# Optimization experiments

Measured on AMD Instinct MI355X. Metric: run time of the kernel, lower is better.

Reference implementation:

```python
import jax, jax.numpy as jnp
import numpy as np

N = 50000        # N_particles
E = 800000       # edges (avg degree 16)
SD = 32          # state_dim = 3 + 2*2 + 25
OC = 16          # message_out_channels
H = 32           # MLP hidden_channels
BN_EPS = 1e-5


def _bn(h, g, b):
    # PyG MLP default BatchNorm1d, training-mode batch stats over rows
    m = h.mean(axis=0)
    v = h.var(axis=0)
    return (h - m) * jax.lax.rsqrt(v + BN_EPS) * g + b


def _mlp3(h, w1, b1, g1, be1, w2, b2, g2, be2, w3, b3):
    # Linear -> BN -> ReLU, Linear -> BN -> ReLU, Linear
    h = jax.nn.relu(_bn(h @ w1 + b1, g1, be1))
    h = jax.nn.relu(_bn(h @ w2 + b2, g2, be2))
    return h @ w3 + b3


def setup_inputs() -> dict:
    key = jax.random.key(0)
    ks = jax.random.split(key, 16)

    def rn(k, shape):
        fan_in = shape[0] if len(shape) > 1 else shape[0]
        return jax.random.normal(k, shape, jnp.float32) / np.sqrt(fan_in)

    inp = {
        "x": jax.random.normal(ks[0], (N, SD), jnp.float32),
        "edge_attr": jax.random.normal(ks[1], (E, SD), jnp.float32),
        "edge_index": jax.random.randint(ks[2], (2, E), 0, N, jnp.int64),
        # edge-weight-generating MLP: SD -> 32 -> 32 -> SD*OC
        "msg_w1": rn(ks[3], (SD, H)), "msg_b1": jnp.zeros((H,), jnp.float32),
        "msg_g1": jnp.ones((H,), jnp.float32), "msg_be1": jnp.zeros((H,), jnp.float32),
        "msg_w2": rn(ks[4], (H, H)), "msg_b2": jnp.zeros((H,), jnp.float32),
        "msg_g2": jnp.ones((H,), jnp.float32), "msg_be2": jnp.zeros((H,), jnp.float32),
        "msg_w3": rn(ks[5], (H, SD * OC)), "msg_b3": jnp.zeros((SD * OC,), jnp.float32),
        # NNConv root weight + bias
        "root_w": rn(ks[6], (SD, OC)), "root_b": jnp.zeros((OC,), jnp.float32),
        # own_state_nn MLP: (SD+OC) -> 32 -> 32 -> SD
        "own_w1": rn(ks[7], (SD + OC, H)), "own_b1": jnp.zeros((H,), jnp.float32),
        "own_g1": jnp.ones((H,), jnp.float32), "own_be1": jnp.zeros((H,), jnp.float32),
        "own_w2": rn(ks[8], (H, H)), "own_b2": jnp.zeros((H,), jnp.float32),
        "own_g2": jnp.ones((H,), jnp.float32), "own_be2": jnp.zeros((H,), jnp.float32),
        "own_w3": rn(ks[9], (H, SD)), "own_b3": jnp.zeros((SD,), jnp.float32),
    }
    return inp


def reference(x, edge_attr, edge_index,
              msg_w1, msg_b1, msg_g1, msg_be1, msg_w2, msg_b2, msg_g2, msg_be2,
              msg_w3, msg_b3, root_w, root_b,
              own_w1, own_b1, own_g1, own_be1, own_w2, own_b2, own_g2, own_be2,
              own_w3, own_b3):
    src, dst = edge_index[0], edge_index[1]
    # per-edge weight matrices: [E, SD, OC]
    W_e = _mlp3(edge_attr, msg_w1, msg_b1, msg_g1, msg_be1,
                msg_w2, msg_b2, msg_g2, msg_be2, msg_w3, msg_b3)
    W_e = W_e.reshape(-1, SD, OC)
    # gather-matmul-scatter (NNConv, aggr='add')
    msg = jnp.einsum('ei,eio->eo', x[src], W_e)          # [E, OC]
    agg = jax.ops.segment_sum(msg, dst, num_segments=N)  # [N, OC]
    messages = agg + x @ root_w + root_b                 # root weight + bias
    combined = jnp.concatenate([x, messages], axis=-1)   # [N, SD+OC]
    new_state = _mlp3(combined, own_w1, own_b1, own_g1, own_be1,
                      own_w2, own_b2, own_g2, own_be2, own_w3, own_b3)
    return new_state
```

## Files before the change

### kernel.cpp

```cpp
#include <hip/hip_runtime.h>
#include <hip/hip_fp16.h>


#define N_NODES 50000
#define N_EDGES 800000
#define SD 32
#define OC 16
#define HID 32
#define BN_EPS 1e-5f
#define NTILES 196

#define OFF_STATS 0u
#define OFF_DEGS  5376u
#define OFF_CURS  205376u
#define OFF_DEGD  405376u
#define OFF_CURD  605376u
#define OFF_BASES 805376u
#define OFF_BASED 1005440u
#define OFF_POSS  1205504u
#define OFF_COMBO 4405504u
#define OFF_AGG   7605504u
#define OFF_H2S   10805504u
#define OFF_MSGB  62005504u

typedef _Float16 f16x8 __attribute__((ext_vector_type(8)));
typedef float f32x16 __attribute__((ext_vector_type(16)));

__device__ __forceinline__ float f4get(const float4& v, int ii) {
  return ii == 0 ? v.x : ii == 1 ? v.y : ii == 2 ? v.z : v.w;
}

__device__ __forceinline__ unsigned pack2(float a, float b) {
  __half2 h = __floats2half2_rn(a, b);
  return *reinterpret_cast<unsigned*>(&h);
}
__device__ __forceinline__ void unpk8(uint4 u, float* o) {
  __half2 a = *reinterpret_cast<__half2*>(&u.x), b = *reinterpret_cast<__half2*>(&u.y);
  __half2 c = *reinterpret_cast<__half2*>(&u.z), d = *reinterpret_cast<__half2*>(&u.w);
  float2 fa = __half22float2(a), fb = __half22float2(b);
  float2 fc = __half22float2(c), fd = __half22float2(d);
  o[0] = fa.x; o[1] = fa.y; o[2] = fb.x; o[3] = fb.y;
  o[4] = fc.x; o[5] = fc.y; o[6] = fd.x; o[7] = fd.y;
}

template<int I4, int IOFF>
__device__ __forceinline__ void mv_acc(const float4* __restrict__ rp,
                                       const float* __restrict__ wlds,
                                       float z[HID]) {
#pragma unroll
  for (int i4 = 0; i4 < I4; ++i4) {
    float4 rv = rp[i4];
#pragma unroll
    for (int ii = 0; ii < 4; ++ii) {
      float s = f4get(rv, ii);
      const float* wrow = wlds + (IOFF + i4 * 4 + ii) * HID;
#pragma unroll
      for (int h4 = 0; h4 < HID / 4; ++h4) {
        float4 wv = *reinterpret_cast<const float4*>(wrow + h4 * 4);
        z[h4 * 4 + 0] = fmaf(s, wv.x, z[h4 * 4 + 0]);
        z[h4 * 4 + 1] = fmaf(s, wv.y, z[h4 * 4 + 1]);
        z[h4 * 4 + 2] = fmaf(s, wv.z, z[h4 * 4 + 2]);
        z[h4 * 4 + 3] = fmaf(s, wv.w, z[h4 * 4 + 3]);
      }
    }
  }
}

__device__ __forceinline__ void mv_reg(const float* __restrict__ v,
                                       const float* __restrict__ wlds,
                                       float z[HID]) {
#pragma unroll
  for (int h = 0; h < HID; ++h) z[h] = 0.f;
#pragma unroll
  for (int i = 0; i < HID; ++i) {
    float s = v[i];
    const float* wrow = wlds + i * HID;
#pragma unroll
    for (int h4 = 0; h4 < HID / 4; ++h4) {
      float4 wv = *reinterpret_cast<const float4*>(wrow + h4 * 4);
      z[h4 * 4 + 0] = fmaf(s, wv.x, z[h4 * 4 + 0]);
      z[h4 * 4 + 1] = fmaf(s, wv.y, z[h4 * 4 + 1]);
      z[h4 * 4 + 2] = fmaf(s, wv.z, z[h4 * 4 + 2]);
      z[h4 * 4 + 3] = fmaf(s, wv.w, z[h4 * 4 + 3]);
    }
  }
}

__device__ __forceinline__ void bn_params(const float* __restrict__ stats, int off,
                                          float cntInv, const float* __restrict__ g,
                                          const float* __restrict__ be,
                                          float* __restrict__ sc, float* __restrict__ sf) {
  if (threadIdx.x < HID) {
    int h = threadIdx.x;
    float mean = stats[off + h] * cntInv;
    float var = stats[off + HID + h] * cntInv - mean * mean;
    float s = g[h] * rsqrtf(var + BN_EPS);
    sc[h] = s;
    sf[h] = fmaf(-mean, s, be[h]);
  }
}

__device__ __forceinline__ void tile_accum(const float z[HID], float* __restrict__ tile,
                                           int h, int g, float& s, float& q) {
  int tid = threadIdx.x;
  __syncthreads();
#pragma unroll
  for (int j = 0; j < HID; ++j) tile[tid * 33 + j] = z[j];
  __syncthreads();
#pragma unroll
  for (int k = 0; k < 32; ++k) {
    float v = tile[(g * 32 + k) * 33 + h];
    s += v;
    q = fmaf(v, v, q);
  }
}

__device__ __forceinline__ void tile_finish(float* __restrict__ tile, int h, int g,
                                            float s, float q,
                                            float* __restrict__ gstats) {
  int tid = threadIdx.x;
  __syncthreads();
  tile[g * 32 + h] = s;
  tile[256 + g * 32 + h] = q;
  __syncthreads();
  if (tid < 64) {
    int hh = tid & 31;
    int base = (tid < 32) ? 0 : 256;
    float acc = 0.f;
#pragma unroll
    for (int g2 = 0; g2 < 8; ++g2) acc += tile[base + g2 * 32 + hh];
    atomicAdd(gstats + ((tid < 32) ? hh : (HID + hh)), acc);
  }
}

__global__ __launch_bounds__(256) void kH(const int* __restrict__ ei,
                                          int* __restrict__ degS, int* __restrict__ degD) {
  int e = blockIdx.x * 256 + threadIdx.x;
  atomicAdd(degS + ei[e], 1);
  atomicAdd(degD + ei[N_EDGES + e], 1);
}

__global__ __launch_bounds__(1024) void kScan(const int* __restrict__ degS, int* __restrict__ baseS,
                                              const int* __restrict__ degD, int* __restrict__ baseD) {
  __shared__ int sc[1024];
  const int* deg = (blockIdx.x == 0) ? degS : degD;
  int* base = (blockIdx.x == 0) ? baseS : baseD;
  int t = threadIdx.x;
  const int C = 49;
  int st = t * C;
  int sum = 0;
  for (int k = 0; k < C; ++k) {
    int i = st + k;
    if (i < N_NODES) sum += deg[i];
  }
  sc[t] = sum;
  __syncthreads();
  for (int s = 1; s < 1024; s <<= 1) {
    int v = (t >= s) ? sc[t - s] : 0;
    __syncthreads();
    sc[t] += v;
    __syncthreads();
  }
  int run = sc[t] - sum;
  for (int k = 0; k < C; ++k) {
    int i = st + k;
    if (i < N_NODES) { base[i] = run; run += deg[i]; }
  }
  if (t == 1023) base[N_NODES] = run;
}

__global__ __launch_bounds__(256) void kRank(const int* __restrict__ ei,
    const int* __restrict__ baseS, const int* __restrict__ baseD,
    int* __restrict__ curS, int* __restrict__ curD,
    int* __restrict__ posS, unsigned* __restrict__ combo) {
  int e = blockIdx.x * 256 + threadIdx.x;
  int s = ei[e], d = ei[N_EDGES + e];
  int rs = atomicAdd(curS + s, 1);
  int ps = baseS[s] + rs;
  posS[e] = ps;
  int rd = atomicAdd(curD + d, 1);
  combo[ps] = (unsigned)(baseD[d] + rd) | ((unsigned)(s & 15) << 27);
}

template<int PHASE>
__global__ __launch_bounds__(256) void sE(
    const float* __restrict__ ea, const int* __restrict__ posS,
    const float* __restrict__ w1, const float* __restrict__ w2,
    const float* __restrict__ g1, const float* __restrict__ be1,
    float* __restrict__ stats, __half* __restrict__ h2s) {
  __shared__ _Float16 xpose[4][32 * 40];
  __shared__ float sred[4][2][32];
  int tid = threadIdx.x;
  int lane = tid & 63, wid = tid >> 6;
  int lr = lane & 31, lh = lane >> 5;

  f16x8 w1h[2], w1l[2], w2h[2], w2l[2];
#pragma unroll
  for (int kf = 0; kf < 2; ++kf) {
#pragma unroll
    for (int j = 0; j < 8; ++j) {
      int k = kf * 16 + lh * 8 + j;
      float v = w1[k * HID + lr];
      _Float16 hi = (_Float16)v;
      w1h[kf][j] = hi;
      w1l[kf][j] = (_Float16)(v - (float)hi);
      if (PHASE == 1) {
        float u = w2[k * HID + lr];
        _Float16 uh = (_Float16)u;
        w2h[kf][j] = uh;
        w2l[kf][j] = (_Float16)(u - (float)uh);
      } else {
        w2h[kf][j] = (_Float16)0.f;
        w2l[kf][j] = (_Float16)0.f;
      }
    }
  }
  float sc1 = 0.f, sf1 = 0.f;
  if (PHASE == 1) {
    float mean = stats[lr] * (1.f / N_EDGES);
    float var = stats[32 + lr] * (1.f / N_EDGES) - mean * mean;
    float s = g1[lr] * rsqrtf(var + BN_EPS);
    sc1 = s;
    sf1 = fmaf(-mean, s, be1[lr]);
  }
  float ssum = 0.f, ssq = 0.f;
  _Float16* xp = xpose[wid];

  for (int t = blockIdx.x * 4 + wid; t < N_EDGES / 32; t += gridDim.x * 4) {
    int e0 = t * 32;
    f16x8 ah[2], al[2];
#pragma unroll
    for (int kf = 0; kf < 2; ++kf) {
      const float4* p = reinterpret_cast<const float4*>(
          ea + (size_t)(e0 + lr) * SD + kf * 16 + lh * 8);
      float4 v0 = p[0], v1 = p[1];
      float vv[8] = {v0.x, v0.y, v0.z, v0.w, v1.x, v1.y, v1.z, v1.w};
#pragma unroll
      for (int j = 0; j < 8; ++j) {
        _Float16 hi = (_Float16)vv[j];
        ah[kf][j] = hi;
        al[kf][j] = (_Float16)(vv[j] - (float)hi);
      }
    }
    f32x16 acc = {};
#pragma unroll
    for (int kf = 0; kf < 2; ++kf) {
      acc = __builtin_amdgcn_mfma_f32_32x32x16_f16(ah[kf], w1h[kf], acc, 0, 0, 0);
      acc = __builtin_amdgcn_mfma_f32_32x32x16_f16(al[kf], w1h[kf], acc, 0, 0, 0);
      acc = __builtin_amdgcn_mfma_f32_32x32x16_f16(ah[kf], w1l[kf], acc, 0, 0, 0);
    }
    if (PHASE == 0) {
#pragma unroll
      for (int r = 0; r < 16; ++r) {
        ssum += acc[r];
        ssq = fmaf(acc[r], acc[r], ssq);
      }
    } else {
#pragma unroll
      for (int r = 0; r < 16; ++r) {
        int row = (r & 3) + 8 * (r >> 2) + 4 * lh;
        float h1 = fmaxf(0.f, fmaf(acc[r], sc1, sf1));
        xp[row * 40 + lr] = (_Float16)h1;
      }
      __builtin_amdgcn_sched_barrier(0);
      asm volatile("s_waitcnt lgkmcnt(0)" ::: "memory");
      __builtin_amdgcn_sched_barrier(0);
      f32x16 acc2 = {};
#pragma unroll
      for (int kf = 0; kf < 2; ++kf) {
        f16x8 a2 = *reinterpret_cast<const f16x8*>(xp + lr * 40 + kf * 16 + lh * 8);
        acc2 = __builtin_amdgcn_mfma_f32_32x32x16_f16(a2, w2h[kf], acc2, 0, 0, 0);
        acc2 = __builtin_amdgcn_mfma_f32_32x32x16_f16(a2, w2l[kf], acc2, 0, 0, 0);
      }
#pragma unroll
      for (int r = 0; r < 16; ++r) {
        ssum += acc2[r];
        ssq = fmaf(acc2[r], acc2[r], ssq);
      }
      __builtin_amdgcn_sched_barrier(0);
      asm volatile("s_waitcnt lgkmcnt(0)" ::: "memory");
      __builtin_amdgcn_sched_barrier(0);
#pragma unroll
      for (int r = 0; r < 16; ++r) {
        int row = (r & 3) + 8 * (r >> 2) + 4 * lh;
        xp[row * 40 + lr] = (_Float16)acc2[r];
      }
      __builtin_amdgcn_sched_barrier(0);
      asm volatile("s_waitcnt lgkmcnt(0)" ::: "memory");
      __builtin_amdgcn_sched_barrier(0);
      int ps = posS[e0 + lr];
      uint4 va = *reinterpret_cast<const uint4*>(xp + lr * 40 + lh * 16);
      uint4 vb = *reinterpret_cast<const uint4*>(xp + lr * 40 + lh * 16 + 8);
      __half* dst = (__half*)h2s + (size_t)ps * HID + lh * 16;
      *reinterpret_cast<uint4*>(dst) = va;
      *reinterpret_cast<uint4*>(dst + 8) = vb;
      __builtin_amdgcn_sched_barrier(0);
    }
  }
  ssum += __shfl_xor(ssum, 32);
  ssq += __shfl_xor(ssq, 32);
  if (lane < 32) {
    sred[wid][0][lane] = ssum;
    sred[wid][1][lane] = ssq;
  }
  __syncthreads();
  if (tid < 64) {
    int h = tid & 31, part = tid >> 5;
    float a = sred[0][part][h] + sred[1][part][h] + sred[2][part][h] + sred[3][part][h];
    atomicAdd(stats + (PHASE == 0 ? 0 : 64) + part * 32 + h, a);
  }
}

__global__ __launch_bounds__(256) void k5_gemm(
    const float* __restrict__ x, const float* __restrict__ w3,
    const float* __restrict__ b3, const unsigned* __restrict__ combo,
    const int* __restrict__ baseS, const __half* __restrict__ h2s,
    const float* __restrict__ stats, const float* __restrict__ g2,
    const float* __restrict__ be2, __half* __restrict__ msgb) {
  __shared__ float Tl[16 * 516];
  __shared__ float xsl[16][33];
  __shared__ float xbl[256];
  __shared__ float b3s[SD * OC];
  __shared__ float sc2[HID], sf2[HID];
  __shared__ int jr[2];
  int tid = threadIdx.x;
  int n0 = blockIdx.x * 16;
  for (int f = tid; f < 16 * SD; f += 256)
    xsl[f >> 5][f & 31] = x[(size_t)n0 * SD + f];
  for (int f = tid; f < SD * OC; f += 256) b3s[f] = b3[f];
  if (tid == 0) jr[0] = baseS[n0];
  if (tid == 1) jr[1] = baseS[n0 + 16];
  bn_params(stats, 64, 1.f / N_EDGES, g2, be2, sc2, sf2);
  __syncthreads();
  {
    int nl = tid >> 4, o = tid & 15;
    float a1 = 0.f;
#pragma unroll
    for (int i = 0; i < SD; ++i) a1 = fmaf(xsl[nl][i], b3s[i * OC + o], a1);
    xbl[tid] = a1;
  }
  {
    int oH = tid & 1, hh = (tid >> 1) & 31, ng = tid >> 6;
    float acc[4][8];
#pragma unroll
    for (int k = 0; k < 4; ++k)
#pragma unroll
      for (int j = 0; j < 8; ++j) acc[k][j] = 0.f;
    const float* wbase = w3 + hh * (SD * OC) + oH * 8;
#pragma unroll
    for (int i = 0; i < SD; ++i) {
      float4 wa = *reinterpret_cast<const float4*>(wbase + i * OC);
      float4 wb = *reinterpret_cast<const float4*>(wbase + i * OC + 4);
#pragma unroll
      for (int k = 0; k < 4; ++k) {
        float xv = xsl[ng * 4 + k][i];
        acc[k][0] = fmaf(xv, wa.x, acc[k][0]);
        acc[k][1] = fmaf(xv, wa.y, acc[k][1]);
        acc[k][2] = fmaf(xv, wa.z, acc[k][2]);
        acc[k][3] = fmaf(xv, wa.w, acc[k][3]);
        acc[k][4] = fmaf(xv, wb.x, acc[k][4]);
        acc[k][5] = fmaf(xv, wb.y, acc[k][5]);
        acc[k][6] = fmaf(xv, wb.z, acc[k][6]);
        acc[k][7] = fmaf(xv, wb.w, acc[k][7]);
      }
    }
#pragma unroll
    for (int k = 0; k < 4; ++k)
#pragma unroll
      for (int jj = 0; jj < 8; ++jj)
        Tl[(ng * 4 + k) * 516 + (oH * 8 + jj) * 32 + hh] = acc[k][jj];
  }
  __syncthreads();
  int jbeg = jr[0], jend = jr[1];
  for (int j = jbeg + tid; j < jend; j += 256) {
    unsigned c = combo[j];
    int dp = (int)(c & 0x07FFFFFFu);
    int nl = (int)(c >> 27);
    const uint4* hp = reinterpret_cast<const uint4*>(h2s + (size_t)j * HID);
    uint4 u0 = hp[0], u1 = hp[1], u2 = hp[2], u3 = hp[3];
    float h2v[HID];
    unpk8(u0, h2v + 0); unpk8(u1, h2v + 8);
    unpk8(u2, h2v + 16); unpk8(u3, h2v + 24);
#pragma unroll
    for (int k = 0; k < HID; ++k) h2v[k] = fmaxf(0.f, fmaf(h2v[k], sc2[k], sf2[k]));
    float m[OC];
#pragma unroll
    for (int o = 0; o < OC; ++o) m[o] = xbl[nl * 16 + o];
#pragma unroll
    for (int o = 0; o < OC; ++o) {
      const float* tb = Tl + nl * 516 + o * 32;
      float a = m[o];
#pragma unroll
      for (int h4 = 0; h4 < 8; ++h4) {
        float4 t = *reinterpret_cast<const float4*>(tb + h4 * 4);
        a = fmaf(h2v[h4 * 4 + 0], t.x, a);
        a = fmaf(h2v[h4 * 4 + 1], t.y, a);
        a = fmaf(h2v[h4 * 4 + 2], t.z, a);
        a = fmaf(h2v[h4 * 4 + 3], t.w, a);
      }
      m[o] = a;
    }
    unsigned us[8];
#pragma unroll
    for (int q = 0; q < 8; ++q) us[q] = pack2(m[2 * q], m[2 * q + 1]);
    uint4* mp = reinterpret_cast<uint4*>(msgb + (size_t)dp * OC);
    mp[0] = make_uint4(us[0], us[1], us[2], us[3]);
    mp[1] = make_uint4(us[4], us[5], us[6], us[7]);
  }
}

__global__ __launch_bounds__(256) void k6_aggr_own(
    const int* __restrict__ baseD, const __half* __restrict__ msgb,
    const float* __restrict__ x, const float* __restrict__ rootw,
    const float* __restrict__ rootb, const float* __restrict__ ow1,
    float* __restrict__ agg, float* __restrict__ stats) {
  __shared__ float xsl[16][33];
  __shared__ float aggl[16 * 17];
  __shared__ float rws[SD * OC];
  __shared__ float ow1s[(SD + OC) * HID];
  __shared__ float zt[16 * 33];
  __shared__ float rbs[OC];
  int tid = threadIdx.x;
  int n0 = blockIdx.x * 16;
  for (int f = tid; f < 16 * SD; f += 256) xsl[f >> 5][f & 31] = x[(size_t)n0 * SD + f];
  for (int f = tid; f < SD * OC; f += 256) rws[f] = rootw[f];
  for (int f = tid; f < (SD + OC) * HID; f += 256) ow1s[f] = ow1[f];
  if (tid < OC) rbs[tid] = rootb[tid];
  __syncthreads();
  int nl = tid >> 4, o = tid & 15;
  int d = n0 + nl;
  float r = rbs[o];
#pragma unroll
  for (int i = 0; i < SD; ++i) r = fmaf(xsl[nl][i], rws[i * OC + o], r);
  int b0 = baseD[d], b1 = baseD[d + 1];
  float s = 0.f;
  for (int j = b0; j < b1; ++j) s += __half2float(msgb[(size_t)j * OC + o]);
  float val = r + s;
  agg[(size_t)d * OC + o] = val;
  aggl[nl * 17 + o] = val;
  __syncthreads();
  float za = 0.f, zb = 0.f;
#pragma unroll
  for (int i = 0; i < SD; ++i) {
    float xv = xsl[nl][i];
    za = fmaf(xv, ow1s[i * HID + o], za);
    zb = fmaf(xv, ow1s[i * HID + o + 16], zb);
  }
#pragma unroll
  for (int i = 0; i < OC; ++i) {
    float mv = aggl[nl * 17 + i];
    za = fmaf(mv, ow1s[(SD + i) * HID + o], za);
    zb = fmaf(mv, ow1s[(SD + i) * HID + o + 16], zb);
  }
  zt[nl * 33 + o] = za;
  zt[nl * 33 + o + 16] = zb;
  __syncthreads();
  if (tid < 64) {
    int h = tid & 31;
    bool issq = tid >= 32;
    float acc = 0.f;
#pragma unroll
    for (int k = 0; k < 16; ++k) {
      float v = zt[k * 33 + h];
      acc += issq ? v * v : v;
    }
    atomicAdd(stats + 128 + (issq ? 32 : 0) + h, acc);
  }
}

__global__ __launch_bounds__(256) void s2_own(
    const float* __restrict__ x, const float* __restrict__ msgs,
    const float* __restrict__ w1, const float* __restrict__ w2,
    const float* __restrict__ g1, const float* __restrict__ be1,
    float* __restrict__ stats) {
  __shared__ float w1s[(SD + OC) * HID], w2s[HID * HID];
  __shared__ float sc1[HID], sf1[HID];
  __shared__ float tile[256 * 33];
  for (int f = threadIdx.x; f < (SD + OC) * HID; f += 256) w1s[f] = w1[f];
  for (int f = threadIdx.x; f < HID * HID; f += 256) w2s[f] = w2[f];
  bn_params(stats, 128, 1.f / N_NODES, g1, be1, sc1, sf1);
  int h = threadIdx.x & 31, g = threadIdx.x >> 5;
  float s = 0.f, q = 0.f;
  __syncthreads();
#pragma unroll 1
  for (int t = blockIdx.x; t < NTILES; t += gridDim.x) {
    int n = t * 256 + threadIdx.x;
    float z2[HID];
#pragma unroll
    for (int j = 0; j < HID; ++j) z2[j] = 0.f;
    if (n < N_NODES) {
      const float4* xp = reinterpret_cast<const float4*>(x + (size_t)n * SD);
      const float4* mp = reinterpret_cast<const float4*>(msgs + (size_t)n * OC);
      float z1[HID];
#pragma unroll
      for (int j = 0; j < HID; ++j) z1[j] = 0.f;
      mv_acc<8, 0>(xp, w1s, z1);
      mv_acc<4, SD>(mp, w1s, z1);
#pragma unroll
      for (int i = 0; i < HID; ++i) z1[i] = fmaxf(0.f, fmaf(z1[i], sc1[i], sf1[i]));
      mv_reg(z1, w2s, z2);
    }
    tile_accum(z2, tile, h, g, s, q);
  }
  tile_finish(tile, h, g, s, q, stats + 192);
}

__global__ __launch_bounds__(256) void k10_own_out(
    const float* __restrict__ x, const float* __restrict__ msgs,
    const float* __restrict__ w1, const float* __restrict__ w2,
    const float* __restrict__ w3o, const float* __restrict__ b3o,
    const float* __restrict__ g1, const float* __restrict__ be1,
    const float* __restrict__ g2, const float* __restrict__ be2,
    const float* __restrict__ stats, float* __restrict__ out) {
  __shared__ float w1s[(SD + OC) * HID], w2s[HID * HID], w3s[HID * SD];
  __shared__ float sc1[HID], sf1[HID], sc2[HID], sf2[HID];
  for (int f = threadIdx.x; f < (SD + OC) * HID; f += 256) w1s[f] = w1[f];
  for (int f = threadIdx.x; f < HID * HID; f += 256) w2s[f] = w2[f];
  for (int f = threadIdx.x; f < HID * SD; f += 256) w3s[f] = w3o[f];
  bn_params(stats, 128, 1.f / N_NODES, g1, be1, sc1, sf1);
  bn_params(stats, 192, 1.f / N_NODES, g2, be2, sc2, sf2);
  __syncthreads();
  int n = blockIdx.x * 256 + threadIdx.x;
  if (n >= N_NODES) return;
  const float4* xp = reinterpret_cast<const float4*>(x + (size_t)n * SD);
  const float4* mp = reinterpret_cast<const float4*>(msgs + (size_t)n * OC);
  float z1[HID];
#pragma unroll
  for (int j = 0; j < HID; ++j) z1[j] = 0.f;
  mv_acc<8, 0>(xp, w1s, z1);
  mv_acc<4, SD>(mp, w1s, z1);
#pragma unroll
  for (int i = 0; i < HID; ++i) z1[i] = fmaxf(0.f, fmaf(z1[i], sc1[i], sf1[i]));
  float z2[HID];
  mv_reg(z1, w2s, z2);
#pragma unroll
  for (int i = 0; i < HID; ++i) z2[i] = fmaxf(0.f, fmaf(z2[i], sc2[i], sf2[i]));
  float z3[HID];
  mv_reg(z2, w3s, z3);
  float4* op = reinterpret_cast<float4*>(out + (size_t)n * SD);
#pragma unroll
  for (int j4 = 0; j4 < 8; ++j4) {
    op[j4] = make_float4(z3[j4 * 4 + 0] + b3o[j4 * 4 + 0],
                         z3[j4 * 4 + 1] + b3o[j4 * 4 + 1],
                         z3[j4 * 4 + 2] + b3o[j4 * 4 + 2],
                         z3[j4 * 4 + 3] + b3o[j4 * 4 + 3]);
  }
}

extern "C" void kernel_launch(void* const* d_in, const int* in_sizes, int n_in,
                              void* d_out, int out_size, void* d_ws, size_t ws_size,
                              hipStream_t stream) {
  const float* x    = (const float*)d_in[0];
  const float* ea   = (const float*)d_in[1];
  const int*   ei   = (const int*)d_in[2];
  const float* mw1  = (const float*)d_in[3];
  const float* mg1  = (const float*)d_in[5];
  const float* mbe1 = (const float*)d_in[6];
  const float* mw2  = (const float*)d_in[7];
  const float* mg2  = (const float*)d_in[9];
  const float* mbe2 = (const float*)d_in[10];
  const float* mw3  = (const float*)d_in[11];
  const float* mb3  = (const float*)d_in[12];
  const float* rw   = (const float*)d_in[13];
  const float* rb   = (const float*)d_in[14];
  const float* ow1  = (const float*)d_in[15];
  const float* og1  = (const float*)d_in[17];
  const float* obe1 = (const float*)d_in[18];
  const float* ow2  = (const float*)d_in[19];
  const float* og2  = (const float*)d_in[21];
  const float* obe2 = (const float*)d_in[22];
  const float* ow3  = (const float*)d_in[23];
  const float* ob3  = (const float*)d_in[24];
  float* out = (float*)d_out;

  char* ws = (char*)d_ws;
  float* stats    = (float*)(ws + OFF_STATS);
  int* degS       = (int*)(ws + OFF_DEGS);
  int* curS       = (int*)(ws + OFF_CURS);
  int* degD       = (int*)(ws + OFF_DEGD);
  int* curD       = (int*)(ws + OFF_CURD);
  int* baseS      = (int*)(ws + OFF_BASES);
  int* baseD      = (int*)(ws + OFF_BASED);
  int* posS       = (int*)(ws + OFF_POSS);
  unsigned* combo = (unsigned*)(ws + OFF_COMBO);
  float* agg      = (float*)(ws + OFF_AGG);
  __half* h2s     = (__half*)(ws + OFF_H2S);
  __half* msgb    = (__half*)(ws + OFF_MSGB);

  hipMemsetAsync(ws, 0, 805376, stream);

  kH<<<3125, 256, 0, stream>>>(ei, degS, degD);
  kScan<<<2, 1024, 0, stream>>>(degS, baseS, degD, baseD);
  kRank<<<3125, 256, 0, stream>>>(ei, baseS, baseD, curS, curD, posS, combo);
  sE<0><<<1024, 256, 0, stream>>>(ea, posS, mw1, mw2, mg1, mbe1, stats, h2s);
  sE<1><<<1024, 256, 0, stream>>>(ea, posS, mw1, mw2, mg1, mbe1, stats, h2s);
  k5_gemm<<<3125, 256, 0, stream>>>(x, mw3, mb3, combo, baseS, h2s,
                                    stats, mg2, mbe2, msgb);
  k6_aggr_own<<<3125, 256, 0, stream>>>(baseD, msgb, x, rw, rb, ow1, agg, stats);
  s2_own<<<NTILES, 256, 0, stream>>>(x, agg, ow1, ow2, og1, obe1, stats);
  k10_own_out<<<(N_NODES + 255) / 256, 256, 0, stream>>>(
      x, agg, ow1, ow2, ow3, ob3, og1, obe1, og2, obe2, stats, out);
}
```

Before: 733.0 us.

## Derive first BN stats from edge_attr Gram matrix; merge rank atomics into histogram pass

```diff
diff --git a/kernel.cpp b/kernel.cpp
--- a/kernel.cpp
+++ b/kernel.cpp
@@ -10,18 +10,20 @@
 #define BN_EPS 1e-5f
 #define NTILES 196
 
-#define OFF_STATS 0u
-#define OFF_DEGS  5376u
-#define OFF_CURS  205376u
-#define OFF_DEGD  405376u
-#define OFF_CURD  605376u
-#define OFF_BASES 805376u
-#define OFF_BASED 1005440u
-#define OFF_POSS  1205504u
-#define OFF_COMBO 4405504u
-#define OFF_AGG   7605504u
-#define OFF_H2S   10805504u
-#define OFF_MSGB  62005504u
+#define OFF_STATS   0u
+#define OFF_MA      1024u
+#define OFF_MB      5120u
+#define OFF_EASUM   9216u
+#define OFF_CURS    9728u
+#define OFF_CURD    209728u
+#define OFF_BASES   409728u
+#define OFF_BASED   609792u
+#define OFF_RANKS   809856u
+#define OFF_RKD_POS 4009856u
+#define OFF_COMBO   7209856u
+#define OFF_AGG     10409856u
+#define OFF_H2S     13609856u
+#define OFF_MSGB    64809856u
 
 typedef _Float16 f16x8 __attribute__((ext_vector_type(8)));
 typedef float f32x16 __attribute__((ext_vector_type(16)));
@@ -133,11 +135,13 @@
   }
 }
 
-__global__ __launch_bounds__(256) void kH(const int* __restrict__ ei,
-                                          int* __restrict__ degS, int* __restrict__ degD) {
+__global__ __launch_bounds__(256) void kR1(const int* __restrict__ ei,
+                                           int* __restrict__ curS, int* __restrict__ curD,
+                                           int* __restrict__ rankS, int* __restrict__ rankD) {
   int e = blockIdx.x * 256 + threadIdx.x;
-  atomicAdd(degS + ei[e], 1);
-  atomicAdd(degD + ei[N_EDGES + e], 1);
+  int s = ei[e], d = ei[N_EDGES + e];
+  rankS[e] = atomicAdd(curS + s, 1);
+  rankD[e] = atomicAdd(curD + d, 1);
 }
 
 __global__ __launch_bounds__(1024) void kScan(const int* __restrict__ degS, int* __restrict__ baseS,
@@ -169,59 +173,155 @@
   if (t == 1023) base[N_NODES] = run;
 }
 
-__global__ __launch_bounds__(256) void kRank(const int* __restrict__ ei,
+__global__ __launch_bounds__(256) void kPre(
+    const float* __restrict__ ea, const int* __restrict__ ei,
     const int* __restrict__ baseS, const int* __restrict__ baseD,
-    int* __restrict__ curS, int* __restrict__ curD,
-    int* __restrict__ posS, unsigned* __restrict__ combo) {
-  int e = blockIdx.x * 256 + threadIdx.x;
-  int s = ei[e], d = ei[N_EDGES + e];
-  int rs = atomicAdd(curS + s, 1);
-  int ps = baseS[s] + rs;
-  posS[e] = ps;
-  int rd = atomicAdd(curD + d, 1);
-  combo[ps] = (unsigned)(baseD[d] + rd) | ((unsigned)(s & 15) << 27);
-}
-
-template<int PHASE>
-__global__ __launch_bounds__(256) void sE(
+    const int* __restrict__ rankS, int* rankD_posS, unsigned* __restrict__ combo,
+    float* __restrict__ MA, float* __restrict__ MB, float* __restrict__ easum) {
+  __shared__ float stg[4][64 * 36];
+  __shared__ float red[4][1024];
+  __shared__ float esred[4][64];
+  int tid = threadIdx.x, lane = tid & 63, wid = tid >> 6;
+  int lr = lane & 31, lh = lane >> 5;
+  f32x16 P = {}, Q = {};
+  float escol = 0.f;
+  for (int t = blockIdx.x; t < N_EDGES / 256; t += gridDim.x) {
+    int e = t * 256 + tid;
+    {
+      int s = ei[e], d = ei[N_EDGES + e];
+      int ps = baseS[s] + rankS[e];
+      int rd = rankD_posS[e];
+      unsigned cb = (unsigned)(baseD[d] + rd) | ((unsigned)(s & 15) << 27);
+      rankD_posS[e] = ps;
+      combo[ps] = cb;
+    }
+    {
+      int eb = t * 256 + 64 * wid;
+      const float4* rp = reinterpret_cast<const float4*>(ea + (size_t)(eb + lane) * SD);
+      float* sp = stg[wid] + lane * 36;
+#pragma unroll
+      for (int u = 0; u < 8; ++u) *reinterpret_cast<float4*>(sp + u * 4) = rp[u];
+      __builtin_amdgcn_sched_barrier(0);
+      asm volatile("s_waitcnt lgkmcnt(0)" ::: "memory");
+      __builtin_amdgcn_sched_barrier(0);
+#pragma unroll
+      for (int rr = 0; rr < 32; ++rr) escol += stg[wid][(32 * lh + rr) * 36 + lr];
+#pragma unroll
+      for (int g = 0; g < 4; ++g) {
+        f16x8 h, lo;
+#pragma unroll
+        for (int j = 0; j < 8; ++j) {
+          float v = stg[wid][(g * 16 + 8 * lh + j) * 36 + lr];
+          _Float16 hi = (_Float16)v;
+          h[j] = hi;
+          lo[j] = (_Float16)(v - (float)hi);
+        }
+        P = __builtin_amdgcn_mfma_f32_32x32x16_f16(h, h, P, 0, 0, 0);
+        Q = __builtin_amdgcn_mfma_f32_32x32x16_f16(h, lo, Q, 0, 0, 0);
+      }
+      __builtin_amdgcn_sched_barrier(0);
+    }
+  }
+  esred[wid][lane] = escol;
+#pragma unroll
+  for (int r = 0; r < 16; ++r) red[wid][r * 64 + lane] = P[r];
+  __syncthreads();
+  float psum[4];
+#pragma unroll
+  for (int u = 0; u < 4; ++u) {
+    int sidx = tid * 4 + u;
+    psum[u] = red[0][sidx] + red[1][sidx] + red[2][sidx] + red[3][sidx];
+  }
+  __syncthreads();
+#pragma unroll
+  for (int r = 0; r < 16; ++r) red[wid][r * 64 + lane] = Q[r];
+  __syncthreads();
+#pragma unroll
+  for (int u = 0; u < 4; ++u) {
+    int sidx = tid * 4 + u;
+    float qs = red[0][sidx] + red[1][sidx] + red[2][sidx] + red[3][sidx];
+    int r = sidx >> 6, l = sidx & 63;
+    int row = (r & 3) + 8 * (r >> 2) + 4 * (l >> 5);
+    int col = l & 31;
+    atomicAdd(MA + row * 32 + col, psum[u] + qs);
+    atomicAdd(MB + row * 32 + col, qs);
+  }
+  if (tid < 32) {
+    float a = 0.f;
+#pragma unroll
+    for (int w = 0; w < 4; ++w) a += esred[w][tid] + esred[w][tid + 32];
+    atomicAdd(easum + tid, a);
+  }
+}
+
+__global__ __launch_bounds__(256) void sE1(
     const float* __restrict__ ea, const int* __restrict__ posS,
     const float* __restrict__ w1, const float* __restrict__ w2,
     const float* __restrict__ g1, const float* __restrict__ be1,
+    const float* __restrict__ MA, const float* __restrict__ MB,
+    const float* __restrict__ easum,
     float* __restrict__ stats, __half* __restrict__ h2s) {
+  __shared__ float MAs[1024], MBs[1024], w1f[1024];
+  __shared__ float parts[32 * 33];
+  __shared__ float easl[32], sc1s[32], sf1s[32];
   __shared__ _Float16 xpose[4][32 * 40];
   __shared__ float sred[4][2][32];
   int tid = threadIdx.x;
   int lane = tid & 63, wid = tid >> 6;
   int lr = lane & 31, lh = lane >> 5;
 
+  for (int f = tid; f < 1024; f += 256) {
+    MAs[f] = MA[f];
+    MBs[f] = MB[f];
+    w1f[f] = w1[f];
+  }
+  if (tid < 32) easl[tid] = easum[tid];
+  __syncthreads();
+  {
+    int h = tid & 31;
+#pragma unroll
+    for (int rep = 0; rep < 4; ++rep) {
+      int i = 8 * rep + (tid >> 5);
+      float tacc = 0.f;
+#pragma unroll
+      for (int j = 0; j < 32; ++j)
+        tacc = fmaf(MAs[i * 32 + j] + MBs[j * 32 + i], w1f[j * 32 + h], tacc);
+      parts[i * 33 + h] = w1f[i * 32 + h] * tacc;
+    }
+  }
+  __syncthreads();
+  if (tid < 32) {
+    int h = tid;
+    float sq = 0.f, sm = 0.f;
+#pragma unroll
+    for (int i = 0; i < 32; ++i) {
+      sq += parts[i * 33 + h];
+      sm = fmaf(easl[i], w1f[i * 32 + h], sm);
+    }
+    float mean = sm * (1.f / N_EDGES);
+    float var = sq * (1.f / N_EDGES) - mean * mean;
+    float s = g1[h] * rsqrtf(var + BN_EPS);
+    sc1s[h] = s;
+    sf1s[h] = fmaf(-mean, s, be1[h]);
+  }
+  __syncthreads();
+  float sc1 = sc1s[lr], sf1 = sf1s[lr];
+
   f16x8 w1h[2], w1l[2], w2h[2], w2l[2];
 #pragma unroll
   for (int kf = 0; kf < 2; ++kf) {
 #pragma unroll
     for (int j = 0; j < 8; ++j) {
       int k = kf * 16 + lh * 8 + j;
-      float v = w1[k * HID + lr];
+      float v = w1f[k * HID + lr];
       _Float16 hi = (_Float16)v;
       w1h[kf][j] = hi;
       w1l[kf][j] = (_Float16)(v - (float)hi);
-      if (PHASE == 1) {
-        float u = w2[k * HID + lr];
-        _Float16 uh = (_Float16)u;
-        w2h[kf][j] = uh;
-        w2l[kf][j] = (_Float16)(u - (float)uh);
-      } else {
-        w2h[kf][j] = (_Float16)0.f;
-        w2l[kf][j] = (_Float16)0.f;
-      }
-    }
-  }
-  float sc1 = 0.f, sf1 = 0.f;
-  if (PHASE == 1) {
-    float mean = stats[lr] * (1.f / N_EDGES);
-    float var = stats[32 + lr] * (1.f / N_EDGES) - mean * mean;
-    float s = g1[lr] * rsqrtf(var + BN_EPS);
-    sc1 = s;
-    sf1 = fmaf(-mean, s, be1[lr]);
+      float u = w2[k * HID + lr];
+      _Float16 uh = (_Float16)u;
+      w2h[kf][j] = uh;
+      w2l[kf][j] = (_Float16)(u - (float)uh);
+    }
   }
   float ssum = 0.f, ssq = 0.f;
   _Float16* xp = xpose[wid];
@@ -249,53 +349,45 @@
       acc = __builtin_amdgcn_mfma_f32_32x32x16_f16(al[kf], w1h[kf], acc, 0, 0, 0);
       acc = __builtin_amdgcn_mfma_f32_32x32x16_f16(ah[kf], w1l[kf], acc, 0, 0, 0);
     }
-    if (PHASE == 0) {
-#pragma unroll
-      for (int r = 0; r < 16; ++r) {
-        ssum += acc[r];
-        ssq = fmaf(acc[r], acc[r], ssq);
-      }
-    } else {
-#pragma unroll
-      for (int r = 0; r < 16; ++r) {
-        int row = (r & 3) + 8 * (r >> 2) + 4 * lh;
-        float h1 = fmaxf(0.f, fmaf(acc[r], sc1, sf1));
-        xp[row * 40 + lr] = (_Float16)h1;
-      }
-      __builtin_amdgcn_sched_barrier(0);
-      asm volatile("s_waitcnt lgkmcnt(0)" ::: "memory");
-      __builtin_amdgcn_sched_barrier(0);
-      f32x16 acc2 = {};
-#pragma unroll
-      for (int kf = 0; kf < 2; ++kf) {
-        f16x8 a2 = *reinterpret_cast<const f16x8*>(xp + lr * 40 + kf * 16 + lh * 8);
-        acc2 = __builtin_amdgcn_mfma_f32_32x32x16_f16(a2, w2h[kf], acc2, 0, 0, 0);
-        acc2 = __builtin_amdgcn_mfma_f32_32x32x16_f16(a2, w2l[kf], acc2, 0, 0, 0);
-      }
-#pragma unroll
-      for (int r = 0; r < 16; ++r) {
-        ssum += acc2[r];
-        ssq = fmaf(acc2[r], acc2[r], ssq);
-      }
-      __builtin_amdgcn_sched_barrier(0);
-      asm volatile("s_waitcnt lgkmcnt(0)" ::: "memory");
-      __builtin_amdgcn_sched_barrier(0);
-#pragma unroll
-      for (int r = 0; r < 16; ++r) {
-        int row = (r & 3) + 8 * (r >> 2) + 4 * lh;
-        xp[row * 40 + lr] = (_Float16)acc2[r];
-      }
-      __builtin_amdgcn_sched_barrier(0);
-      asm volatile("s_waitcnt lgkmcnt(0)" ::: "memory");
-      __builtin_amdgcn_sched_barrier(0);
-      int ps = posS[e0 + lr];
-      uint4 va = *reinterpret_cast<const uint4*>(xp + lr * 40 + lh * 16);
-      uint4 vb = *reinterpret_cast<const uint4*>(xp + lr * 40 + lh * 16 + 8);
-      __half* dst = (__half*)h2s + (size_t)ps * HID + lh * 16;
-      *reinterpret_cast<uint4*>(dst) = va;
-      *reinterpret_cast<uint4*>(dst + 8) = vb;
-      __builtin_amdgcn_sched_barrier(0);
-    }
+#pragma unroll
+    for (int r = 0; r < 16; ++r) {
+      int row = (r & 3) + 8 * (r >> 2) + 4 * lh;
+      float h1 = fmaxf(0.f, fmaf(acc[r], sc1, sf1));
+      xp[row * 40 + lr] = (_Float16)h1;
+    }
+    __builtin_amdgcn_sched_barrier(0);
+    asm volatile("s_waitcnt lgkmcnt(0)" ::: "memory");
+    __builtin_amdgcn_sched_barrier(0);
+    f32x16 acc2 = {};
+#pragma unroll
+    for (int kf = 0; kf < 2; ++kf) {
+      f16x8 a2 = *reinterpret_cast<const f16x8*>(xp + lr * 40 + kf * 16 + lh * 8);
+      acc2 = __builtin_amdgcn_mfma_f32_32x32x16_f16(a2, w2h[kf], acc2, 0, 0, 0);
+      acc2 = __builtin_amdgcn_mfma_f32_32x32x16_f16(a2, w2l[kf], acc2, 0, 0, 0);
+    }
+#pragma unroll
+    for (int r = 0; r < 16; ++r) {
+      ssum += acc2[r];
+      ssq = fmaf(acc2[r], acc2[r], ssq);
+    }
+    __builtin_amdgcn_sched_barrier(0);
+    asm volatile("s_waitcnt lgkmcnt(0)" ::: "memory");
+    __builtin_amdgcn_sched_barrier(0);
+#pragma unroll
+    for (int r = 0; r < 16; ++r) {
+      int row = (r & 3) + 8 * (r >> 2) + 4 * lh;
+      xp[row * 40 + lr] = (_Float16)acc2[r];
+    }
+    __builtin_amdgcn_sched_barrier(0);
+    asm volatile("s_waitcnt lgkmcnt(0)" ::: "memory");
+    __builtin_amdgcn_sched_barrier(0);
+    int ps = posS[e0 + lr];
+    uint4 va = *reinterpret_cast<const uint4*>(xp + lr * 40 + lh * 16);
+    uint4 vb = *reinterpret_cast<const uint4*>(xp + lr * 40 + lh * 16 + 8);
+    __half* dst = (__half*)h2s + (size_t)ps * HID + lh * 16;
+    *reinterpret_cast<uint4*>(dst) = va;
+    *reinterpret_cast<uint4*>(dst + 8) = vb;
+    __builtin_amdgcn_sched_barrier(0);
   }
   ssum += __shfl_xor(ssum, 32);
   ssq += __shfl_xor(ssq, 32);
@@ -307,7 +399,7 @@
   if (tid < 64) {
     int h = tid & 31, part = tid >> 5;
     float a = sred[0][part][h] + sred[1][part][h] + sred[2][part][h] + sred[3][part][h];
-    atomicAdd(stats + (PHASE == 0 ? 0 : 64) + part * 32 + h, a);
+    atomicAdd(stats + 64 + part * 32 + h, a);
   }
 }
 
@@ -575,25 +667,28 @@
 
   char* ws = (char*)d_ws;
   float* stats    = (float*)(ws + OFF_STATS);
-  int* degS       = (int*)(ws + OFF_DEGS);
+  float* MA       = (float*)(ws + OFF_MA);
+  float* MB       = (float*)(ws + OFF_MB);
+  float* easum    = (float*)(ws + OFF_EASUM);
   int* curS       = (int*)(ws + OFF_CURS);
-  int* degD       = (int*)(ws + OFF_DEGD);
   int* curD       = (int*)(ws + OFF_CURD);
   int* baseS      = (int*)(ws + OFF_BASES);
   int* baseD      = (int*)(ws + OFF_BASED);
-  int* posS       = (int*)(ws + OFF_POSS);
+  int* rankS      = (int*)(ws + OFF_RANKS);
+  int* rankD_posS = (int*)(ws + OFF_RKD_POS);
   unsigned* combo = (unsigned*)(ws + OFF_COMBO);
   float* agg      = (float*)(ws + OFF_AGG);
   __half* h2s     = (__half*)(ws + OFF_H2S);
   __half* msgb    = (__half*)(ws + OFF_MSGB);
 
-  hipMemsetAsync(ws, 0, 805376, stream);
-
-  kH<<<3125, 256, 0, stream>>>(ei, degS, degD);
-  kScan<<<2, 1024, 0, stream>>>(degS, baseS, degD, baseD);
-  kRank<<<3125, 256, 0, stream>>>(ei, baseS, baseD, curS, curD, posS, combo);
-  sE<0><<<1024, 256, 0, stream>>>(ea, posS, mw1, mw2, mg1, mbe1, stats, h2s);
-  sE<1><<<1024, 256, 0, stream>>>(ea, posS, mw1, mw2, mg1, mbe1, stats, h2s);
+  hipMemsetAsync(ws, 0, 409728, stream);
+
+  kR1<<<3125, 256, 0, stream>>>(ei, curS, curD, rankS, rankD_posS);
+  kScan<<<2, 1024, 0, stream>>>(curS, baseS, curD, baseD);
+  kPre<<<512, 256, 0, stream>>>(ea, ei, baseS, baseD, rankS, rankD_posS, combo,
+                                MA, MB, easum);
+  sE1<<<1024, 256, 0, stream>>>(ea, rankD_posS, mw1, mw2, mg1, mbe1,
+                                MA, MB, easum, stats, h2s);
   k5_gemm<<<3125, 256, 0, stream>>>(x, mw3, mb3, combo, baseS, h2s,
                                     stats, mg2, mbe2, msgb);
   k6_aggr_own<<<3125, 256, 0, stream>>>(baseD, msgb, x, rw, rb, ow1, agg, stats);
```

Measured after the change: 711.9 us. -2.9%, faster.
